# Performance work log

Hardware: AMD Instinct MI355X
Metric: run time of the kernel (lower is better)

Reference implementation:

```python
import jax, jax.numpy as jnp
import numpy as np

MARGIN = 0.1
SCALE_POS = 2.0
SCALE_NEG = 50.0
THRESH = 0.5
EPS = 1e-5


def setup_inputs() -> dict:
    key = jax.random.key(0)
    k1, k2 = jax.random.split(key)
    feats = jax.random.normal(k1, (4096, 2, 192), dtype=jnp.float32)
    labels = jax.random.randint(k2, (4096,), 0, 4096, dtype=jnp.int64)
    return {"feats": feats, "labels": labels}


def reference(feats, labels):
    B, n_utt, D = feats.shape
    lab = jnp.repeat(labels, n_utt)            # [N]
    f = feats.reshape(-1, D)                   # [N, D]
    N = f.shape[0]

    sim = f @ f.T                              # [N, N]
    # F.normalize(sim): L2-normalize each row, eps=1e-12
    row_norm = jnp.maximum(jnp.linalg.norm(sim, axis=1, keepdims=True), 1e-12)
    S = sim / row_norm

    same = lab[None, :] == lab[:, None]        # [N, N]
    pos_mask = same & (S < 1.0 - EPS)          # pos_pair_ (includes self if < 1-eps)
    neg_mask = ~same                           # neg_pair_

    min_pos = jnp.min(jnp.where(pos_mask, S, jnp.inf), axis=1)    # per-row min(pos_pair_)
    max_neg = jnp.max(jnp.where(neg_mask, S, -jnp.inf), axis=1)   # per-row max(neg_pair_)

    neg_keep = neg_mask & (S > (min_pos - MARGIN)[:, None])
    pos_keep = pos_mask & (S < (max_neg + MARGIN)[:, None])

    has_neg = jnp.any(neg_keep, axis=1)
    has_pos = jnp.any(pos_keep, axis=1)
    valid = has_neg & has_pos

    pos_sum = jnp.sum(jnp.where(pos_keep, jnp.exp(-SCALE_POS * (S - THRESH)), 0.0), axis=1)
    neg_sum = jnp.sum(jnp.where(neg_keep, jnp.exp(SCALE_NEG * (S - THRESH)), 0.0), axis=1)

    row_loss = (1.0 / SCALE_POS) * jnp.log1p(pos_sum) + (1.0 / SCALE_NEG) * jnp.log1p(neg_sum)
    loss = jnp.sum(jnp.where(valid, row_loss, 0.0)) / N

    # prec1 = percent of rows skipped for having no surviving negatives
    prec1 = jnp.sum(~has_neg).astype(jnp.float32) * 100.0 / N
    return loss, prec1
```

## Files before the change

kernel.cpp:

```cpp
#include <hip/hip_runtime.h>
#include <math.h>

typedef float  f32x4  __attribute__((ext_vector_type(4)));
typedef int    int4v  __attribute__((ext_vector_type(4)));
typedef int    int8v  __attribute__((ext_vector_type(8)));

constexpr float MARGIN    = 0.1f;
constexpr float SCALE_POS = 2.0f;
constexpr float SCALE_NEG = 50.0f;
constexpr float THRESH    = 0.5f;
constexpr float ONE_EPS   = 1.0f - 1e-5f;
constexpr float LOG2E     = 1.4426950408889634f;
constexpr float BC        = -(SCALE_NEG * THRESH * LOG2E);
constexpr float VCUT_COEF = (36.0674f - 30.0f) / (SCALE_NEG * LOG2E);

constexpr int D      = 192;
constexpr int KP     = 256;
constexpr int RT     = 4;
constexpr int RPW    = 64;
constexpr int RPB    = 256;
constexpr int CSPLIT = 16;

constexpr int TILE_B8 = 4096;
constexpr int SCALE1  = 0x7f7f7f7f;

__device__ inline float fast_exp2(float x) {
#if __has_builtin(__builtin_amdgcn_exp2f)
  return __builtin_amdgcn_exp2f(x);
#else
  return exp2f(x);
#endif
}

__device__ inline void pin_frag8(int8v& v) {
  asm volatile("" : "+v"(v));
}

__global__ __launch_bounds__(1024) void k_prep(
    const float* __restrict__ f, unsigned char* __restrict__ pk8, int nrows,
    const int* __restrict__ labs, int* __restrict__ hist_g, int* __restrict__ offs_g,
    int* __restrict__ bucket, float* __restrict__ accum, int n)
{
  if (blockIdx.x < 64) {
    int gid = blockIdx.x * 1024 + threadIdx.x;
    int r = gid >> 3, j = gid & 7;
    if (r >= nrows) return;
    float x[32];
    if (j < 6) {
      const float* src = f + (size_t)r * D + j * 32;
#pragma unroll
      for (int i = 0; i < 8; ++i) {
        float4 v = *(const float4*)(src + i * 4);
        x[i * 4 + 0] = v.x; x[i * 4 + 1] = v.y; x[i * 4 + 2] = v.z; x[i * 4 + 3] = v.w;
      }
    } else {
#pragma unroll
      for (int i = 0; i < 32; ++i) x[i] = 0.f;
    }
    union { int s[8]; int8v v; } u;
#pragma unroll
    for (int i = 0; i < 8; ++i) {
      int p = __builtin_amdgcn_cvt_pk_fp8_f32(x[i * 4 + 0], x[i * 4 + 1], 0, false);
      p     = __builtin_amdgcn_cvt_pk_fp8_f32(x[i * 4 + 2], x[i * 4 + 3], p, true);
      u.s[i] = p;
    }
    int tile = r >> 4, c = r & 15, g = j >> 2, qq = j & 3;
    *(int8v*)(pk8 + (size_t)tile * TILE_B8 + g * 2048 + (qq * 16 + c) * 32) = u.v;
    return;
  }

  __shared__ int histL[4096];
  __shared__ int offsL[4096];
  __shared__ int scanb[1024];
  const int t = threadIdx.x;

  if (t < 3) accum[t] = 0.f;
  for (int i = t; i < 4096; i += 1024) histL[i] = 0;
  __syncthreads();
  for (int i = t; i < n; i += 1024) atomicAdd(&histL[labs[i]], 1);
  __syncthreads();
  int base = t * 4;
  int v[4]; int ls = 0;
  for (int k = 0; k < 4; ++k) { v[k] = ls; ls += histL[base + k]; }
  scanb[t] = ls;
  __syncthreads();
  for (int o = 1; o < 1024; o <<= 1) {
    int x = (t >= o) ? scanb[t - o] : 0;
    __syncthreads();
    scanb[t] += x;
    __syncthreads();
  }
  int ebase = scanb[t] - ls;
  for (int k = 0; k < 4; ++k) {
    offsL[base + k] = ebase + v[k];
    offs_g[base + k] = ebase + v[k];
    hist_g[base + k] = histL[base + k];
  }
  __syncthreads();
  for (int i = t; i < 4096; i += 1024) histL[i] = 0;
  __syncthreads();
  for (int i = t; i < n; i += 1024) {
    int lab = labs[i];
    int p = atomicAdd(&histL[lab], 1);
    bucket[offsL[lab] + p] = i;
  }
}

__global__ __launch_bounds__(256, 2) void k_pass1(
    const unsigned char* __restrict__ pk8, const int* __restrict__ labs,
    float* __restrict__ sumsqP, float* __restrict__ maxnegP,
    int N, int cps)
{
  __shared__ int ldsLab[512];

  const int tid  = threadIdx.x;
  const int lane = tid & 63;
  const int w    = tid >> 6;
  const int q    = lane >> 4;
  const int c    = lane & 15;
  const int cs   = blockIdx.x & (CSPLIT - 1);
  const int rbb  = blockIdx.x / CSPLIT;
  const int rowbase = rbb * RPB + w * RPW;
  const int col0 = cs * cps;
  const int ctile0 = col0 >> 4;
  const int ntiles = cps >> 4;

  for (int i = tid; i < cps; i += 256) ldsLab[i] = labs[(col0 + i) >> 1];

  int8v afr[RT][2];
#pragma unroll
  for (int rt = 0; rt < RT; ++rt)
#pragma unroll
    for (int g = 0; g < 2; ++g) {
      afr[rt][g] = *(const int8v*)(pk8 + (size_t)((rowbase >> 4) + rt) * TILE_B8 + g * 2048 + lane * 32);
      pin_frag8(afr[rt][g]);
    }

  int labrow[RT][4];
#pragma unroll
  for (int rt = 0; rt < RT; ++rt)
#pragma unroll
    for (int rr = 0; rr < 4; ++rr)
      labrow[rt][rr] = labs[(rowbase + rt * 16 + q * 4 + rr) >> 1];

  float ssq[RT][4], mxn[RT][4];
#pragma unroll
  for (int rt = 0; rt < RT; ++rt)
#pragma unroll
    for (int rr = 0; rr < 4; ++rr) { ssq[rt][rr] = 0.f; mxn[rt][rr] = -INFINITY; }

  __syncthreads();

  auto loadB = [&](int tile, int8v (&bf)[2]) {
    const unsigned char* bp = pk8 + (size_t)(ctile0 + tile) * TILE_B8 + lane * 32;
#pragma unroll
    for (int g = 0; g < 2; ++g) bf[g] = *(const int8v*)(bp + g * 2048);
  };
  auto compute = [&](const int8v (&bf)[2], int t) {
    const int labcol = ldsLab[t * 16 + c];
    f32x4 acc[RT];
#pragma unroll
    for (int rt = 0; rt < RT; ++rt) acc[rt] = 0.f;
#pragma unroll
    for (int g = 0; g < 2; ++g)
#pragma unroll
      for (int rt = 0; rt < RT; ++rt)
        acc[rt] = __builtin_amdgcn_mfma_scale_f32_16x16x128_f8f6f4(
            afr[rt][g], bf[g], acc[rt], 0, 0, 0, SCALE1, 0, SCALE1);
#pragma unroll
    for (int rt = 0; rt < RT; ++rt)
#pragma unroll
      for (int rr = 0; rr < 4; ++rr) {
        float v = acc[rt][rr];
        ssq[rt][rr] = fmaf(v, v, ssq[rt][rr]);
        float vm = (labrow[rt][rr] == labcol) ? -INFINITY : v;
        mxn[rt][rr] = fmaxf(mxn[rt][rr], vm);
      }
  };

  auto wrap = [&](int x) { return (x < ntiles) ? x : 0; };
  int8v b0[2], b1[2], b2[2], b3[2];
  loadB(0, b0);
  loadB(1, b1);
  for (int t = 0; t < ntiles; t += 4) {
    loadB(wrap(t + 2), b2); compute(b0, t);
    loadB(wrap(t + 3), b3); compute(b1, t + 1);
    loadB(wrap(t + 4), b0); compute(b2, t + 2);
    loadB(wrap(t + 5), b1); compute(b3, t + 3);
  }

#pragma unroll
  for (int rt = 0; rt < RT; ++rt)
#pragma unroll
    for (int rr = 0; rr < 4; ++rr) {
      float s = ssq[rt][rr], m = mxn[rt][rr];
#pragma unroll
      for (int msk = 1; msk < 16; msk <<= 1) {
        s += __shfl_xor(s, msk, 64);
        m = fmaxf(m, __shfl_xor(m, msk, 64));
      }
      if (c == 0) {
        int row = rowbase + rt * 16 + q * 4 + rr;
        sumsqP[(size_t)cs * N + row] = s;
        maxnegP[(size_t)cs * N + row] = m;
      }
    }
}

__global__ void k_rowstats(
    const float* __restrict__ f, const int* __restrict__ labs,
    const float* __restrict__ sumsqP, const float* __restrict__ maxnegP,
    const int* __restrict__ offs, const int* __restrict__ hist, const int* __restrict__ bucket,
    float* __restrict__ nthr2, float* __restrict__ arow,
    float* __restrict__ validf, float* __restrict__ hasnegf, float* __restrict__ posloss,
    int N)
{
  const int lane = threadIdx.x & 63;
  const int row  = blockIdx.x * 4 + (threadIdx.x >> 6);

  float s = 0.f, m = -INFINITY;
  if (lane < CSPLIT) {
    s = sumsqP[(size_t)lane * N + row];
    m = maxnegP[(size_t)lane * N + row];
  }
#pragma unroll
  for (int msk = 1; msk < 64; msk <<= 1) {
    s += __shfl_xor(s, msk, 64);
    m = fmaxf(m, __shfl_xor(m, msk, 64));
  }
  float nrm = fmaxf(sqrtf(s), 1e-12f);
  float inv = 1.0f / nrm;
  float maxnegS = m * inv;
  float posth = fminf(ONE_EPS, maxnegS + MARGIN);

  const int lab = labs[row >> 1];
  const int beg = offs[lab], cnt = hist[lab];
  const float* fi = f + (size_t)row * D;
  float x0 = fi[lane], x1 = fi[lane + 64], x2 = fi[lane + 128];

  float minp = INFINITY, psum = 0.f; int pcnt = 0;
  for (int t = 0; t < cnt; ++t) {
    int smp = bucket[beg + t];
#pragma unroll
    for (int u = 0; u < 2; ++u) {
      const float* fj = f + (size_t)(smp * 2 + u) * D;
      float p = x0 * fj[lane] + x1 * fj[lane + 64] + x2 * fj[lane + 128];
#pragma unroll
      for (int msk = 1; msk < 64; msk <<= 1) p += __shfl_xor(p, msk, 64);
      minp = fminf(minp, p);
      float S = p * inv;
      if (S < posth) {
        psum += fast_exp2((THRESH - S) * (SCALE_POS * LOG2E));
        pcnt++;
      }
    }
  }

  float minS = minp * inv;
  float min_pos = (minS < ONE_EPS) ? minS : INFINITY;
  bool hneg = maxnegS > (min_pos - MARGIN);
  bool valid = hneg && (pcnt > 0);
  if (lane == 0) {
    nthr2[row]   = fmaxf((min_pos - MARGIN) * nrm, VCUT_COEF * nrm);
    arow[row]    = inv * (SCALE_NEG * LOG2E);
    validf[row]  = valid ? 1.f : 0.f;
    hasnegf[row] = hneg ? 1.f : 0.f;
    posloss[row] = valid ? ((1.0f / SCALE_POS) * log1pf(psum)) : 0.f;
  }
}

__global__ __launch_bounds__(256, 2) void k_pass2(
    const unsigned char* __restrict__ pk8,
    const float* __restrict__ nthr2, const float* __restrict__ arow,
    const float* __restrict__ maxnegP,
    float* __restrict__ negsumP, int N, int cps)
{
  const int lane = threadIdx.x & 63;
  const int w    = threadIdx.x >> 6;
  const int q    = lane >> 4;
  const int c    = lane & 15;
  const int cs   = blockIdx.x & (CSPLIT - 1);
  const int rbb  = blockIdx.x / CSPLIT;
  const int rowbase = rbb * RPB + w * RPW;
  const int ctile0 = (cs * cps) >> 4;
  const int ntiles = cps >> 4;

  {
    int myrow = rowbase + lane;
    float mn = maxnegP[(size_t)cs * N + myrow];
    float th = nthr2[myrow];
    unsigned long long bal = __ballot(mn > th);
    if (bal == 0ull) {
      negsumP[(size_t)cs * N + myrow] = 0.f;
      return;
    }
  }

  int8v afr[RT][2];
#pragma unroll
  for (int rt = 0; rt < RT; ++rt)
#pragma unroll
    for (int g = 0; g < 2; ++g) {
      afr[rt][g] = *(const int8v*)(pk8 + (size_t)((rowbase >> 4) + rt) * TILE_B8 + g * 2048 + lane * 32);
      pin_frag8(afr[rt][g]);
    }

  float nthrv[RT][4], arw[RT][4], ns[RT][4];
#pragma unroll
  for (int rt = 0; rt < RT; ++rt)
#pragma unroll
    for (int rr = 0; rr < 4; ++rr) {
      int row = rowbase + rt * 16 + q * 4 + rr;
      nthrv[rt][rr] = nthr2[row];
      arw[rt][rr]   = arow[row];
      ns[rt][rr]    = 0.f;
    }

  auto loadB = [&](int tile, int8v (&bf)[2]) {
    const unsigned char* bp = pk8 + (size_t)(ctile0 + tile) * TILE_B8 + lane * 32;
#pragma unroll
    for (int g = 0; g < 2; ++g) bf[g] = *(const int8v*)(bp + g * 2048);
  };
  auto compute = [&](const int8v (&bf)[2]) {
    f32x4 acc[RT];
#pragma unroll
    for (int rt = 0; rt < RT; ++rt) acc[rt] = 0.f;
#pragma unroll
    for (int g = 0; g < 2; ++g)
#pragma unroll
      for (int rt = 0; rt < RT; ++rt)
        acc[rt] = __builtin_amdgcn_mfma_scale_f32_16x16x128_f8f6f4(
            afr[rt][g], bf[g], acc[rt], 0, 0, 0, SCALE1, 0, SCALE1);
#pragma unroll
    for (int rt = 0; rt < RT; ++rt)
#pragma unroll
      for (int rr = 0; rr < 4; ++rr) {
        float v = acc[rt][rr];
        float e = fast_exp2(fmaf(v, arw[rt][rr], BC));
        ns[rt][rr] += (v > nthrv[rt][rr]) ? e : 0.f;
      }
  };

  int8v b0[2], b1[2];
  loadB(0, b0);
  for (int t = 0; t < ntiles; t += 2) {
    loadB(t + 1, b1);
    compute(b0);
    int nx = t + 2; nx = (nx < ntiles) ? nx : 0;
    loadB(nx, b0);
    compute(b1);
  }

#pragma unroll
  for (int rt = 0; rt < RT; ++rt)
#pragma unroll
    for (int rr = 0; rr < 4; ++rr) {
      float sv = ns[rt][rr];
#pragma unroll
      for (int msk = 1; msk < 16; msk <<= 1) sv += __shfl_xor(sv, msk, 64);
      if (c == 0) {
        int row = rowbase + rt * 16 + q * 4 + rr;
        negsumP[(size_t)cs * N + row] = sv;
      }
    }
}

__global__ void k_final(const float* __restrict__ negsumP, const float* __restrict__ posloss,
                        const float* __restrict__ validf, const float* __restrict__ hasnegf,
                        float* __restrict__ accum, float* __restrict__ out, int N)
{
  int i = blockIdx.x * blockDim.x + threadIdx.x;
  float lacc = 0.f, nacc = 0.f;
  if (i < N) {
    float nsum = 0.f;
    for (int cs2 = 0; cs2 < CSPLIT; ++cs2) nsum += negsumP[(size_t)cs2 * N + i];
    lacc = validf[i] * (posloss[i] + (1.0f / SCALE_NEG) * log1pf(nsum));
    nacc = 1.0f - hasnegf[i];
  }
#pragma unroll
  for (int msk = 1; msk < 64; msk <<= 1) {
    lacc += __shfl_xor(lacc, msk, 64);
    nacc += __shfl_xor(nacc, msk, 64);
  }
  __shared__ float sl[4], sn[4];
  __shared__ bool isLast;
  int wid = threadIdx.x >> 6, lane = threadIdx.x & 63;
  if (lane == 0) { sl[wid] = lacc; sn[wid] = nacc; }
  __syncthreads();
  if (threadIdx.x == 0) {
    float L = sl[0] + sl[1] + sl[2] + sl[3];
    float Nn = sn[0] + sn[1] + sn[2] + sn[3];
    atomicAdd(&accum[0], L);
    atomicAdd(&accum[1], Nn);
    __threadfence();
    int tkt = atomicAdd((int*)&accum[2], 1);
    isLast = (tkt == (int)gridDim.x - 1);
  }
  __syncthreads();
  if (isLast && threadIdx.x == 0) {
    __threadfence();
    out[0] = accum[0] / (float)N;
    out[1] = accum[1] * 100.0f / (float)N;
  }
}

extern "C" void kernel_launch(void* const* d_in, const int* in_sizes, int n_in,
                              void* d_out, int out_size, void* d_ws, size_t ws_size,
                              hipStream_t stream)
{
  (void)n_in; (void)out_size; (void)ws_size;
  const float* f    = (const float*)d_in[0];
  const int*   labs = (const int*)d_in[1];
  const int Bs = in_sizes[1];
  const int N  = 2 * Bs;

  char* ws = (char*)d_ws;
  size_t off = 0;
  auto alloc = [&](size_t bytes) -> void* {
    void* p = ws + off;
    off += (bytes + 255) & ~(size_t)255;
    return p;
  };
  unsigned char* pk8 = (unsigned char*)alloc((size_t)N * KP);
  float* sumsqP  = (float*)alloc((size_t)CSPLIT * N * sizeof(float));
  float* maxnegP = (float*)alloc((size_t)CSPLIT * N * sizeof(float));
  float* negsumP = (float*)alloc((size_t)CSPLIT * N * sizeof(float));
  float* nthr2   = (float*)alloc((size_t)N * sizeof(float));
  float* arow    = (float*)alloc((size_t)N * sizeof(float));
  float* validf  = (float*)alloc((size_t)N * sizeof(float));
  float* hasnegf = (float*)alloc((size_t)N * sizeof(float));
  float* posloss = (float*)alloc((size_t)N * sizeof(float));
  int* hist   = (int*)alloc((size_t)Bs * sizeof(int));
  int* offs   = (int*)alloc((size_t)Bs * sizeof(int));
  int* bucket = (int*)alloc((size_t)Bs * sizeof(int));
  float* accum = (float*)alloc(4 * sizeof(float));

  k_prep<<<65, 1024, 0, stream>>>(f, pk8, N, labs, hist, offs, bucket, accum, Bs);

  const int cps   = N / CSPLIT;
  const int grid1 = (N / RPB) * CSPLIT;
  k_pass1<<<grid1, 256, 0, stream>>>(pk8, labs, sumsqP, maxnegP, N, cps);
  k_rowstats<<<N / 4, 256, 0, stream>>>(f, labs, sumsqP, maxnegP, offs, hist, bucket,
                                        nthr2, arow, validf, hasnegf, posloss, N);
  k_pass2<<<grid1, 256, 0, stream>>>(pk8, nthr2, arow, maxnegP, negsumP, N, cps);
  k_final<<<N / 256, 256, 0, stream>>>(negsumP, posloss, validf, hasnegf, accum, (float*)d_out, N);
}
```

Before: 100.4 us.

## Sort rows by label, use range masks, and fold final reduction into pass2

```diff
diff --git a/kernel.cpp b/kernel.cpp
--- a/kernel.cpp
+++ b/kernel.cpp
@@ -23,6 +23,7 @@
 
 constexpr int TILE_B8 = 4096;
 constexpr int SCALE1  = 0x7f7f7f7f;
+constexpr int FLAG_MAGIC = 0x1357beef;
 
 __device__ inline float fast_exp2(float x) {
 #if __has_builtin(__builtin_amdgcn_exp2f)
@@ -38,81 +39,95 @@
 
 __global__ __launch_bounds__(1024) void k_prep(
     const float* __restrict__ f, unsigned char* __restrict__ pk8, int nrows,
-    const int* __restrict__ labs, int* __restrict__ hist_g, int* __restrict__ offs_g,
-    int* __restrict__ bucket, float* __restrict__ accum, int n)
+    const int* __restrict__ labs, int* __restrict__ bucket,
+    int* __restrict__ rowperm, int* __restrict__ rowlo, int* __restrict__ rowhi,
+    float* __restrict__ accum, int n)
 {
-  if (blockIdx.x < 64) {
-    int gid = blockIdx.x * 1024 + threadIdx.x;
-    int r = gid >> 3, j = gid & 7;
-    if (r >= nrows) return;
-    float x[32];
-    if (j < 6) {
-      const float* src = f + (size_t)r * D + j * 32;
-#pragma unroll
-      for (int i = 0; i < 8; ++i) {
-        float4 v = *(const float4*)(src + i * 4);
-        x[i * 4 + 0] = v.x; x[i * 4 + 1] = v.y; x[i * 4 + 2] = v.z; x[i * 4 + 3] = v.w;
-      }
-    } else {
-#pragma unroll
-      for (int i = 0; i < 32; ++i) x[i] = 0.f;
-    }
-    union { int s[8]; int8v v; } u;
+  int* flag = (int*)&accum[3];
+  if (blockIdx.x == 64) {
+    __shared__ int histL[4096];
+    __shared__ int offsL[4097];
+    __shared__ int scanb[1024];
+    const int t = threadIdx.x;
+    if (t < 3) accum[t] = 0.f;
+    for (int i = t; i < 4096; i += 1024) histL[i] = 0;
+    __syncthreads();
+    for (int i = t; i < n; i += 1024) atomicAdd(&histL[labs[i]], 1);
+    __syncthreads();
+    int base = t * 4;
+    int v[4]; int ls = 0;
+    for (int k = 0; k < 4; ++k) { v[k] = ls; ls += histL[base + k]; }
+    scanb[t] = ls;
+    __syncthreads();
+    for (int o = 1; o < 1024; o <<= 1) {
+      int x = (t >= o) ? scanb[t - o] : 0;
+      __syncthreads();
+      scanb[t] += x;
+      __syncthreads();
+    }
+    int ebase = scanb[t] - ls;
+    for (int k = 0; k < 4; ++k) offsL[base + k] = ebase + v[k];
+    if (t == 0) offsL[4096] = n;
+    __syncthreads();
+    for (int i = t; i < 4096; i += 1024) histL[i] = 0;
+    __syncthreads();
+    for (int i = t; i < n; i += 1024) {
+      int lab = labs[i];
+      int p = atomicAdd(&histL[lab], 1);
+      int slot = offsL[lab] + p;
+      bucket[slot] = i;
+      int lo = 2 * offsL[lab];
+      int hi = 2 * offsL[lab + 1];
+      rowperm[slot * 2]     = i * 2;
+      rowperm[slot * 2 + 1] = i * 2 + 1;
+      rowlo[slot * 2] = lo; rowlo[slot * 2 + 1] = lo;
+      rowhi[slot * 2] = hi; rowhi[slot * 2 + 1] = hi;
+    }
+    __threadfence();
+    __syncthreads();
+    if (t == 0)
+      __hip_atomic_store(flag, FLAG_MAGIC, __ATOMIC_RELEASE, __HIP_MEMORY_SCOPE_AGENT);
+    return;
+  }
+
+  if (threadIdx.x == 0) {
+    while (__hip_atomic_load(flag, __ATOMIC_ACQUIRE, __HIP_MEMORY_SCOPE_AGENT) != FLAG_MAGIC)
+      __builtin_amdgcn_s_sleep(2);
+  }
+  __syncthreads();
+  int gid = blockIdx.x * 1024 + threadIdx.x;
+  int prow = gid >> 3, j = gid & 7;
+  if (prow >= nrows) return;
+  int src = rowperm[prow];
+  float x[32];
+  if (j < 6) {
+    const float* sp = f + (size_t)src * D + j * 32;
 #pragma unroll
     for (int i = 0; i < 8; ++i) {
-      int p = __builtin_amdgcn_cvt_pk_fp8_f32(x[i * 4 + 0], x[i * 4 + 1], 0, false);
-      p     = __builtin_amdgcn_cvt_pk_fp8_f32(x[i * 4 + 2], x[i * 4 + 3], p, true);
-      u.s[i] = p;
-    }
-    int tile = r >> 4, c = r & 15, g = j >> 2, qq = j & 3;
-    *(int8v*)(pk8 + (size_t)tile * TILE_B8 + g * 2048 + (qq * 16 + c) * 32) = u.v;
-    return;
-  }
-
-  __shared__ int histL[4096];
-  __shared__ int offsL[4096];
-  __shared__ int scanb[1024];
-  const int t = threadIdx.x;
-
-  if (t < 3) accum[t] = 0.f;
-  for (int i = t; i < 4096; i += 1024) histL[i] = 0;
-  __syncthreads();
-  for (int i = t; i < n; i += 1024) atomicAdd(&histL[labs[i]], 1);
-  __syncthreads();
-  int base = t * 4;
-  int v[4]; int ls = 0;
-  for (int k = 0; k < 4; ++k) { v[k] = ls; ls += histL[base + k]; }
-  scanb[t] = ls;
-  __syncthreads();
-  for (int o = 1; o < 1024; o <<= 1) {
-    int x = (t >= o) ? scanb[t - o] : 0;
-    __syncthreads();
-    scanb[t] += x;
-    __syncthreads();
-  }
-  int ebase = scanb[t] - ls;
-  for (int k = 0; k < 4; ++k) {
-    offsL[base + k] = ebase + v[k];
-    offs_g[base + k] = ebase + v[k];
-    hist_g[base + k] = histL[base + k];
-  }
-  __syncthreads();
-  for (int i = t; i < 4096; i += 1024) histL[i] = 0;
-  __syncthreads();
-  for (int i = t; i < n; i += 1024) {
-    int lab = labs[i];
-    int p = atomicAdd(&histL[lab], 1);
-    bucket[offsL[lab] + p] = i;
-  }
+      float4 v = *(const float4*)(sp + i * 4);
+      x[i * 4 + 0] = v.x; x[i * 4 + 1] = v.y; x[i * 4 + 2] = v.z; x[i * 4 + 3] = v.w;
+    }
+  } else {
+#pragma unroll
+    for (int i = 0; i < 32; ++i) x[i] = 0.f;
+  }
+  union { int s[8]; int8v v; } u;
+#pragma unroll
+  for (int i = 0; i < 8; ++i) {
+    int p = __builtin_amdgcn_cvt_pk_fp8_f32(x[i * 4 + 0], x[i * 4 + 1], 0, false);
+    p     = __builtin_amdgcn_cvt_pk_fp8_f32(x[i * 4 + 2], x[i * 4 + 3], p, true);
+    u.s[i] = p;
+  }
+  int tile = prow >> 4, c = prow & 15, g = j >> 2, qq = j & 3;
+  *(int8v*)(pk8 + (size_t)tile * TILE_B8 + g * 2048 + (qq * 16 + c) * 32) = u.v;
 }
 
 __global__ __launch_bounds__(256, 2) void k_pass1(
-    const unsigned char* __restrict__ pk8, const int* __restrict__ labs,
+    const unsigned char* __restrict__ pk8,
+    const int* __restrict__ rowlo, const int* __restrict__ rowhi,
     float* __restrict__ sumsqP, float* __restrict__ maxnegP,
     int N, int cps)
 {
-  __shared__ int ldsLab[512];
-
   const int tid  = threadIdx.x;
   const int lane = tid & 63;
   const int w    = tid >> 6;
@@ -125,8 +140,6 @@
   const int ctile0 = col0 >> 4;
   const int ntiles = cps >> 4;
 
-  for (int i = tid; i < cps; i += 256) ldsLab[i] = labs[(col0 + i) >> 1];
-
   int8v afr[RT][2];
 #pragma unroll
   for (int rt = 0; rt < RT; ++rt)
@@ -136,20 +149,21 @@
       pin_frag8(afr[rt][g]);
     }
 
-  int labrow[RT][4];
+  int lov[RT][4], hiv[RT][4];
 #pragma unroll
   for (int rt = 0; rt < RT; ++rt)
 #pragma unroll
-    for (int rr = 0; rr < 4; ++rr)
-      labrow[rt][rr] = labs[(rowbase + rt * 16 + q * 4 + rr) >> 1];
+    for (int rr = 0; rr < 4; ++rr) {
+      int prow = rowbase + rt * 16 + q * 4 + rr;
+      lov[rt][rr] = rowlo[prow];
+      hiv[rt][rr] = rowhi[prow];
+    }
 
   float ssq[RT][4], mxn[RT][4];
 #pragma unroll
   for (int rt = 0; rt < RT; ++rt)
 #pragma unroll
     for (int rr = 0; rr < 4; ++rr) { ssq[rt][rr] = 0.f; mxn[rt][rr] = -INFINITY; }
-
-  __syncthreads();
 
   auto loadB = [&](int tile, int8v (&bf)[2]) {
     const unsigned char* bp = pk8 + (size_t)(ctile0 + tile) * TILE_B8 + lane * 32;
@@ -157,7 +171,7 @@
     for (int g = 0; g < 2; ++g) bf[g] = *(const int8v*)(bp + g * 2048);
   };
   auto compute = [&](const int8v (&bf)[2], int t) {
-    const int labcol = ldsLab[t * 16 + c];
+    const int p = col0 + t * 16 + c;
     f32x4 acc[RT];
 #pragma unroll
     for (int rt = 0; rt < RT; ++rt) acc[rt] = 0.f;
@@ -173,20 +187,20 @@
       for (int rr = 0; rr < 4; ++rr) {
         float v = acc[rt][rr];
         ssq[rt][rr] = fmaf(v, v, ssq[rt][rr]);
-        float vm = (labrow[rt][rr] == labcol) ? -INFINITY : v;
+        bool same = (p >= lov[rt][rr]) && (p < hiv[rt][rr]);
+        float vm = same ? -INFINITY : v;
         mxn[rt][rr] = fmaxf(mxn[rt][rr], vm);
       }
   };
 
-  auto wrap = [&](int x) { return (x < ntiles) ? x : 0; };
-  int8v b0[2], b1[2], b2[2], b3[2];
+  int8v b0[2], b1[2];
   loadB(0, b0);
-  loadB(1, b1);
-  for (int t = 0; t < ntiles; t += 4) {
-    loadB(wrap(t + 2), b2); compute(b0, t);
-    loadB(wrap(t + 3), b3); compute(b1, t + 1);
-    loadB(wrap(t + 4), b0); compute(b2, t + 2);
-    loadB(wrap(t + 5), b1); compute(b3, t + 3);
+  for (int t = 0; t < ntiles; t += 2) {
+    loadB(t + 1, b1);
+    compute(b0, t);
+    int nx = t + 2; nx = (nx < ntiles) ? nx : 0;
+    loadB(nx, b0);
+    compute(b1, t + 1);
   }
 
 #pragma unroll
@@ -200,17 +214,18 @@
         m = fmaxf(m, __shfl_xor(m, msk, 64));
       }
       if (c == 0) {
-        int row = rowbase + rt * 16 + q * 4 + rr;
-        sumsqP[(size_t)cs * N + row] = s;
-        maxnegP[(size_t)cs * N + row] = m;
+        int prow = rowbase + rt * 16 + q * 4 + rr;
+        sumsqP[(size_t)cs * N + prow] = s;
+        maxnegP[(size_t)cs * N + prow] = m;
       }
     }
 }
 
 __global__ void k_rowstats(
-    const float* __restrict__ f, const int* __restrict__ labs,
+    const float* __restrict__ f,
+    const int* __restrict__ rowperm, const int* __restrict__ rowlo, const int* __restrict__ rowhi,
+    const int* __restrict__ bucket,
     const float* __restrict__ sumsqP, const float* __restrict__ maxnegP,
-    const int* __restrict__ offs, const int* __restrict__ hist, const int* __restrict__ bucket,
     float* __restrict__ nthr2, float* __restrict__ arow,
     float* __restrict__ validf, float* __restrict__ hasnegf, float* __restrict__ posloss,
     int N)
@@ -233,14 +248,14 @@
   float maxnegS = m * inv;
   float posth = fminf(ONE_EPS, maxnegS + MARGIN);
 
-  const int lab = labs[row >> 1];
-  const int beg = offs[lab], cnt = hist[lab];
-  const float* fi = f + (size_t)row * D;
+  const int orig = rowperm[row];
+  const int s0 = rowlo[row] >> 1, s1 = rowhi[row] >> 1;
+  const float* fi = f + (size_t)orig * D;
   float x0 = fi[lane], x1 = fi[lane + 64], x2 = fi[lane + 128];
 
   float minp = INFINITY, psum = 0.f; int pcnt = 0;
-  for (int t = 0; t < cnt; ++t) {
-    int smp = bucket[beg + t];
+  for (int t = s0; t < s1; ++t) {
+    int smp = bucket[t];
 #pragma unroll
     for (int u = 0; u < 2; ++u) {
       const float* fj = f + (size_t)(smp * 2 + u) * D;
@@ -273,7 +288,11 @@
     const unsigned char* __restrict__ pk8,
     const float* __restrict__ nthr2, const float* __restrict__ arow,
     const float* __restrict__ maxnegP,
-    float* __restrict__ negsumP, int N, int cps)
+    float* __restrict__ negsumP,
+    const float* __restrict__ posloss, const float* __restrict__ validf,
+    const float* __restrict__ hasnegf,
+    float* __restrict__ accum, float* __restrict__ out,
+    int N, int cps)
 {
   const int lane = threadIdx.x & 63;
   const int w    = threadIdx.x >> 6;
@@ -285,97 +304,102 @@
   const int ctile0 = (cs * cps) >> 4;
   const int ntiles = cps >> 4;
 
+  bool skip;
   {
     int myrow = rowbase + lane;
     float mn = maxnegP[(size_t)cs * N + myrow];
     float th = nthr2[myrow];
     unsigned long long bal = __ballot(mn > th);
-    if (bal == 0ull) {
-      negsumP[(size_t)cs * N + myrow] = 0.f;
-      return;
-    }
-  }
-
-  int8v afr[RT][2];
-#pragma unroll
-  for (int rt = 0; rt < RT; ++rt)
-#pragma unroll
-    for (int g = 0; g < 2; ++g) {
-      afr[rt][g] = *(const int8v*)(pk8 + (size_t)((rowbase >> 4) + rt) * TILE_B8 + g * 2048 + lane * 32);
-      pin_frag8(afr[rt][g]);
-    }
-
-  float nthrv[RT][4], arw[RT][4], ns[RT][4];
-#pragma unroll
-  for (int rt = 0; rt < RT; ++rt)
-#pragma unroll
-    for (int rr = 0; rr < 4; ++rr) {
-      int row = rowbase + rt * 16 + q * 4 + rr;
-      nthrv[rt][rr] = nthr2[row];
-      arw[rt][rr]   = arow[row];
-      ns[rt][rr]    = 0.f;
-    }
-
-  auto loadB = [&](int tile, int8v (&bf)[2]) {
-    const unsigned char* bp = pk8 + (size_t)(ctile0 + tile) * TILE_B8 + lane * 32;
-#pragma unroll
-    for (int g = 0; g < 2; ++g) bf[g] = *(const int8v*)(bp + g * 2048);
-  };
-  auto compute = [&](const int8v (&bf)[2]) {
-    f32x4 acc[RT];
-#pragma unroll
-    for (int rt = 0; rt < RT; ++rt) acc[rt] = 0.f;
-#pragma unroll
-    for (int g = 0; g < 2; ++g)
+    skip = (bal == 0ull);
+    if (skip) negsumP[(size_t)cs * N + myrow] = 0.f;
+  }
+
+  if (!skip) {
+    int8v afr[RT][2];
+#pragma unroll
+    for (int rt = 0; rt < RT; ++rt)
+#pragma unroll
+      for (int g = 0; g < 2; ++g) {
+        afr[rt][g] = *(const int8v*)(pk8 + (size_t)((rowbase >> 4) + rt) * TILE_B8 + g * 2048 + lane * 32);
+        pin_frag8(afr[rt][g]);
+      }
+
+    float nthrv[RT][4], arw[RT][4], ns[RT][4];
+#pragma unroll
+    for (int rt = 0; rt < RT; ++rt)
+#pragma unroll
+      for (int rr = 0; rr < 4; ++rr) {
+        int row = rowbase + rt * 16 + q * 4 + rr;
+        nthrv[rt][rr] = nthr2[row];
+        arw[rt][rr]   = arow[row];
+        ns[rt][rr]    = 0.f;
+      }
+
+    auto loadB = [&](int tile, int8v (&bf)[2]) {
+      const unsigned char* bp = pk8 + (size_t)(ctile0 + tile) * TILE_B8 + lane * 32;
+#pragma unroll
+      for (int g = 0; g < 2; ++g) bf[g] = *(const int8v*)(bp + g * 2048);
+    };
+    auto compute = [&](const int8v (&bf)[2]) {
+      f32x4 acc[RT];
+#pragma unroll
+      for (int rt = 0; rt < RT; ++rt) acc[rt] = 0.f;
+#pragma unroll
+      for (int g = 0; g < 2; ++g)
+#pragma unroll
+        for (int rt = 0; rt < RT; ++rt)
+          acc[rt] = __builtin_amdgcn_mfma_scale_f32_16x16x128_f8f6f4(
+              afr[rt][g], bf[g], acc[rt], 0, 0, 0, SCALE1, 0, SCALE1);
 #pragma unroll
       for (int rt = 0; rt < RT; ++rt)
-        acc[rt] = __builtin_amdgcn_mfma_scale_f32_16x16x128_f8f6f4(
-            afr[rt][g], bf[g], acc[rt], 0, 0, 0, SCALE1, 0, SCALE1);
+#pragma unroll
+        for (int rr = 0; rr < 4; ++rr) {
+          float v = acc[rt][rr];
+          float e = fast_exp2(fmaf(v, arw[rt][rr], BC));
+          ns[rt][rr] += (v > nthrv[rt][rr]) ? e : 0.f;
+        }
+    };
+
+    int8v b0[2], b1[2];
+    loadB(0, b0);
+    for (int t = 0; t < ntiles; t += 2) {
+      loadB(t + 1, b1);
+      compute(b0);
+      int nx = t + 2; nx = (nx < ntiles) ? nx : 0;
+      loadB(nx, b0);
+      compute(b1);
+    }
+
 #pragma unroll
     for (int rt = 0; rt < RT; ++rt)
 #pragma unroll
       for (int rr = 0; rr < 4; ++rr) {
-        float v = acc[rt][rr];
-        float e = fast_exp2(fmaf(v, arw[rt][rr], BC));
-        ns[rt][rr] += (v > nthrv[rt][rr]) ? e : 0.f;
-      }
-  };
-
-  int8v b0[2], b1[2];
-  loadB(0, b0);
-  for (int t = 0; t < ntiles; t += 2) {
-    loadB(t + 1, b1);
-    compute(b0);
-    int nx = t + 2; nx = (nx < ntiles) ? nx : 0;
-    loadB(nx, b0);
-    compute(b1);
-  }
-
-#pragma unroll
-  for (int rt = 0; rt < RT; ++rt)
-#pragma unroll
-    for (int rr = 0; rr < 4; ++rr) {
-      float sv = ns[rt][rr];
-#pragma unroll
-      for (int msk = 1; msk < 16; msk <<= 1) sv += __shfl_xor(sv, msk, 64);
-      if (c == 0) {
-        int row = rowbase + rt * 16 + q * 4 + rr;
-        negsumP[(size_t)cs * N + row] = sv;
-      }
-    }
-}
-
-__global__ void k_final(const float* __restrict__ negsumP, const float* __restrict__ posloss,
-                        const float* __restrict__ validf, const float* __restrict__ hasnegf,
-                        float* __restrict__ accum, float* __restrict__ out, int N)
-{
-  int i = blockIdx.x * blockDim.x + threadIdx.x;
+        float sv = ns[rt][rr];
+#pragma unroll
+        for (int msk = 1; msk < 16; msk <<= 1) sv += __shfl_xor(sv, msk, 64);
+        if (c == 0) {
+          int row = rowbase + rt * 16 + q * 4 + rr;
+          negsumP[(size_t)cs * N + row] = sv;
+        }
+      }
+  }
+
+  __threadfence();
+  __syncthreads();
+  __shared__ bool isLast;
+  if (threadIdx.x == 0) {
+    int tkt = atomicAdd((int*)&accum[2], 1);
+    isLast = (tkt == (int)gridDim.x - 1);
+  }
+  __syncthreads();
+  if (!isLast) return;
+
   float lacc = 0.f, nacc = 0.f;
-  if (i < N) {
+  for (int i = threadIdx.x; i < N; i += 256) {
     float nsum = 0.f;
     for (int cs2 = 0; cs2 < CSPLIT; ++cs2) nsum += negsumP[(size_t)cs2 * N + i];
-    lacc = validf[i] * (posloss[i] + (1.0f / SCALE_NEG) * log1pf(nsum));
-    nacc = 1.0f - hasnegf[i];
+    lacc += validf[i] * (posloss[i] + (1.0f / SCALE_NEG) * log1pf(nsum));
+    nacc += 1.0f - hasnegf[i];
   }
 #pragma unroll
   for (int msk = 1; msk < 64; msk <<= 1) {
@@ -383,24 +407,14 @@
     nacc += __shfl_xor(nacc, msk, 64);
   }
   __shared__ float sl[4], sn[4];
-  __shared__ bool isLast;
-  int wid = threadIdx.x >> 6, lane = threadIdx.x & 63;
-  if (lane == 0) { sl[wid] = lacc; sn[wid] = nacc; }
+  int wid = threadIdx.x >> 6;
+  if ((threadIdx.x & 63) == 0) { sl[wid] = lacc; sn[wid] = nacc; }
   __syncthreads();
   if (threadIdx.x == 0) {
-    float L = sl[0] + sl[1] + sl[2] + sl[3];
+    float L  = sl[0] + sl[1] + sl[2] + sl[3];
     float Nn = sn[0] + sn[1] + sn[2] + sn[3];
-    atomicAdd(&accum[0], L);
-    atomicAdd(&accum[1], Nn);
-    __threadfence();
-    int tkt = atomicAdd((int*)&accum[2], 1);
-    isLast = (tkt == (int)gridDim.x - 1);
-  }
-  __syncthreads();
-  if (isLast && threadIdx.x == 0) {
-    __threadfence();
-    out[0] = accum[0] / (float)N;
-    out[1] = accum[1] * 100.0f / (float)N;
+    out[0] = L / (float)N;
+    out[1] = Nn * 100.0f / (float)N;
   }
 }
 
@@ -430,18 +444,19 @@
   float* validf  = (float*)alloc((size_t)N * sizeof(float));
   float* hasnegf = (float*)alloc((size_t)N * sizeof(float));
   float* posloss = (float*)alloc((size_t)N * sizeof(float));
-  int* hist   = (int*)alloc((size_t)Bs * sizeof(int));
-  int* offs   = (int*)alloc((size_t)Bs * sizeof(int));
-  int* bucket = (int*)alloc((size_t)Bs * sizeof(int));
+  int* bucket  = (int*)alloc((size_t)Bs * sizeof(int));
+  int* rowperm = (int*)alloc((size_t)N * sizeof(int));
+  int* rowlo   = (int*)alloc((size_t)N * sizeof(int));
+  int* rowhi   = (int*)alloc((size_t)N * sizeof(int));
   float* accum = (float*)alloc(4 * sizeof(float));
 
-  k_prep<<<65, 1024, 0, stream>>>(f, pk8, N, labs, hist, offs, bucket, accum, Bs);
+  k_prep<<<65, 1024, 0, stream>>>(f, pk8, N, labs, bucket, rowperm, rowlo, rowhi, accum, Bs);
 
   const int cps   = N / CSPLIT;
   const int grid1 = (N / RPB) * CSPLIT;
-  k_pass1<<<grid1, 256, 0, stream>>>(pk8, labs, sumsqP, maxnegP, N, cps);
-  k_rowstats<<<N / 4, 256, 0, stream>>>(f, labs, sumsqP, maxnegP, offs, hist, bucket,
+  k_pass1<<<grid1, 256, 0, stream>>>(pk8, rowlo, rowhi, sumsqP, maxnegP, N, cps);
+  k_rowstats<<<N / 4, 256, 0, stream>>>(f, rowperm, rowlo, rowhi, bucket, sumsqP, maxnegP,
                                         nthr2, arow, validf, hasnegf, posloss, N);
-  k_pass2<<<grid1, 256, 0, stream>>>(pk8, nthr2, arow, maxnegP, negsumP, N, cps);
-  k_final<<<N / 256, 256, 0, stream>>>(negsumP, posloss, validf, hasnegf, accum, (float*)d_out, N);
-}
+  k_pass2<<<grid1, 256, 0, stream>>>(pk8, nthr2, arow, maxnegP, negsumP,
+                                     posloss, validf, hasnegf, accum, (float*)d_out, N, cps);
+}
```

Result: slower. 196.3 us (+95.6%).
